# Performance work log

Measured on AMD Instinct MI355X. Metric: run time of the kernel, lower is better.

The kernel has to match this reference:

```python
import jax, jax.numpy as jnp
import numpy as np

N_T = 8
N_R = 2
NOISE = 1e-12  # 10**(-120/10)
B = 65536


def setup_inputs() -> dict:
    key = jax.random.key(0)
    ks = jax.random.split(key, 7)
    return {
        "theta1": jax.random.normal(ks[0], (B, 264), dtype=jnp.float32),
        "G1r": jax.random.normal(ks[1], (B, N_R, 100), dtype=jnp.float32),
        "G1i": jax.random.normal(ks[2], (B, N_R, 100), dtype=jnp.float32),
        "G2r": jax.random.normal(ks[3], (B, N_R, 100), dtype=jnp.float32),
        "G2i": jax.random.normal(ks[4], (B, N_R, 100), dtype=jnp.float32),
        "Ur": jax.random.normal(ks[5], (B, 100, N_T), dtype=jnp.float32),
        "Ui": jax.random.normal(ks[6], (B, 100, N_T), dtype=jnp.float32),
    }


def _rate(phi, Fsig, Fintf):
    # phi: [B, N_r, N_t], Fsig/Fintf: [B, N_t, N_r]
    A = jnp.einsum("bnt,btr->bnr", phi, Fsig)    # signal term  [B, N_r, N_r]
    C = jnp.einsum("bnt,btr->bnr", phi, Fintf)   # interference [B, N_r, N_r]
    # Mu = C C^H + noise (elementwise scalar add, faithful to torch source)
    Mu = jnp.einsum("bnr,bmr->bnm", C, jnp.conj(C)) + NOISE
    inner = jnp.einsum("brn,bnm,bms->brs", jnp.conj(A).transpose(0, 2, 1) if False else jnp.conj(jnp.swapaxes(A, 1, 2)), jnp.linalg.inv(Mu), A)
    # note: torch does 1 + matrix (elementwise), not identity add
    return jnp.real(jnp.log(jnp.linalg.det(1.0 + inner)))  # [B]


def reference(theta1, G1r, G1i, G2r, G2i, Ur, Ui):
    M1N1 = N_T * N_R  # 16
    F1 = theta1[:, 200:200 + M1N1] + 1j * theta1[:, 200 + M1N1:200 + 2 * M1N1]
    F2 = theta1[:, 200 + 2 * M1N1:200 + 3 * M1N1] + 1j * theta1[:, 200 + 3 * M1N1:]
    # power normalization: F * sqrt(2 / (F^H F))
    F1 = F1 * jnp.sqrt(2.0 / jnp.sum(jnp.conj(F1) * F1, axis=1, keepdims=True))
    F2 = F2 * jnp.sqrt(2.0 / jnp.sum(jnp.conj(F2) * F2, axis=1, keepdims=True))
    F1m = F1.reshape(-1, N_T, N_R)
    F2m = F2.reshape(-1, N_T, N_R)

    theta = theta1[:, 0:100] + 1j * theta1[:, 100:200]  # [B, 100]
    G1 = G1r + 1j * G1i
    G2 = G2r + 1j * G2i
    U = Ur + 1j * Ui

    # phi = G @ diag(theta) @ U, vectorized over batch
    phi1 = jnp.einsum("bnk,bk,bkt->bnt", G1, theta, U)  # [B, N_r, N_t]
    phi2 = jnp.einsum("bnk,bk,bkt->bnt", G2, theta, U)

    R1 = _rate(phi1, F1m, F2m)
    R2 = _rate(phi2, F2m, F1m)
    R = jnp.maximum(-R1, -R2)
    return jnp.sum(R) / theta1.shape[0]
```

## Files before the change

kernel.cpp:

```cpp
#include <hip/hip_runtime.h>
#include <math.h>

#define NOISE 1e-12f
#define WSZ 1064
#define WSZ4 266

__device__ __forceinline__ float2 cmul(float2 a, float2 b) {
    return make_float2(a.x*b.x - a.y*b.y, a.x*b.y + a.y*b.x);
}
__device__ __forceinline__ float2 cconjmul(float2 a, float2 b) {
    return make_float2(a.x*b.x + a.y*b.y, a.x*b.y - a.y*b.x);
}
__device__ __forceinline__ float2 cmulconj(float2 a, float2 b) {
    return make_float2(a.x*b.x + a.y*b.y, a.y*b.x - a.x*b.y);
}
__device__ __forceinline__ float2 cadd(float2 a, float2 b){ return make_float2(a.x+b.x, a.y+b.y); }
__device__ __forceinline__ float2 csub(float2 a, float2 b){ return make_float2(a.x-b.x, a.y-b.y); }
__device__ __forceinline__ float2 cscale(float s, float2 a){ return make_float2(s*a.x, s*a.y); }

typedef const void __attribute__((address_space(1)))* gas_t;
typedef void __attribute__((address_space(3)))* las_t;
__device__ __forceinline__ void gll16(const float* g, float* l) {
    __builtin_amdgcn_global_load_lds((gas_t)g, (las_t)l, 16, 0, 0);
}

__global__ __launch_bounds__(256) void rate_kernel(
    const float* __restrict__ t1,
    const float* __restrict__ G1r, const float* __restrict__ G1i,
    const float* __restrict__ G2r, const float* __restrict__ G2i,
    const float* __restrict__ Ur,  const float* __restrict__ Ui,
    float* __restrict__ partial)
{
    __shared__ float4 lds4[4 * 2 * WSZ4];
    __shared__ float2 ent[4][4][16];
    __shared__ float wsum[4];
    const int wave = threadIdx.x >> 6;
    const int lane = threadIdx.x & 63;
    const int t  = lane & 7;
    const int k0 = lane >> 3;
    const int e8 = k0;
    const int nn = (e8 >> 1) & 1;
    const int rr = e8 & 1;
    float* Wbuf = (float*)(lds4 + wave * 2 * WSZ4);

    #define STAGE(dst, bb) {                                                  \
        const float* tb_ = t1 + (long)(bb) * 264;                             \
        gll16(tb_ + lane * 4, (dst));                        \
        if (lane < 2)  gll16(tb_ + 256 + lane * 4, (dst) + 256);              \
        if (lane < 50) {                                                      \
            gll16(G1r + (long)(bb) * 200 + lane * 4, (dst) + 264);            \
            gll16(G1i + (long)(bb) * 200 + lane * 4, (dst) + 464);            \
            gll16(G2r + (long)(bb) * 200 + lane * 4, (dst) + 664);            \
            gll16(G2i + (long)(bb) * 200 + lane * 4, (dst) + 864);            \
        }                                                                     \
    }

    const long bbase = (long)blockIdx.x * 16 + (long)wave * 4;
    STAGE(Wbuf, bbase);

    const float* urb = Ur + bbase * 800;
    const float* uib = Ui + bbase * 800;
    const int uoff = 32 * k0 + t;
    #define LDU2(idx) make_float2(urb[(idx)], uib[(idx)])

    float2 u0 = LDU2(uoff), u1 = LDU2(uoff+8), u2 = LDU2(uoff+16), u3 = LDU2(uoff+24);

    #define CMATH(thr,thi, ar,ai, cr,ci, dr,di, er,ei, u) {      \
        float wr = (thr)*(u).x - (thi)*(u).y;                    \
        float wi = (thr)*(u).y + (thi)*(u).x;                    \
        p[0] += (ar)*wr - (ai)*wi;  p[1] += (ar)*wi + (ai)*wr;   \
        p[2] += (cr)*wr - (ci)*wi;  p[3] += (cr)*wi + (ci)*wr;   \
        p[4] += (dr)*wr - (di)*wi;  p[5] += (dr)*wi + (di)*wr;   \
        p[6] += (er)*wr - (ei)*wi;  p[7] += (er)*wi + (ei)*wr; }

    #define JGROUP(q, U0, U1, U2, U3) {                                   \
        float4 tr  = F4[(q)];        float4 ti  = F4[25  + (q)];          \
        float4 a0r = F4[66  + (q)];  float4 a0i = F4[116 + (q)];          \
        float4 a1r = F4[91  + (q)];  float4 a1i = F4[141 + (q)];          \
        float4 b0r = F4[166 + (q)];  float4 b0i = F4[216 + (q)];          \
        float4 b1r = F4[191 + (q)];  float4 b1i = F4[241 + (q)];          \
        CMATH(tr.x,ti.x, a0r.x,a0i.x, a1r.x,a1i.x, b0r.x,b0i.x, b1r.x,b1i.x, U0); \
        CMATH(tr.y,ti.y, a0r.y,a0i.y, a1r.y,a1i.y, b0r.y,b0i.y, b1r.y,b1i.y, U1); \
        CMATH(tr.z,ti.z, a0r.z,a0i.z, a1r.z,a1i.z, b0r.z,b0i.z, b1r.z,b1i.z, U2); \
        CMATH(tr.w,ti.w, a0r.w,a0i.w, a1r.w,a1i.w, b0r.w,b0i.w, b1r.w,b1i.w, U3); }

    for (int it = 0; it < 4; ++it) {
        float* W = Wbuf + (it & 1) * WSZ;
        const float4* F4 = (const float4*)W;

        if (it < 3) {
            STAGE(Wbuf + ((it + 1) & 1) * WSZ, bbase + it + 1);
            asm volatile("s_waitcnt vmcnt(14)" ::: "memory");
        }
        __builtin_amdgcn_sched_barrier(0);

        float p[8] = {0,0,0,0,0,0,0,0};

        #pragma unroll 1
        for (int j = 0; j < 3; ++j) {
            float2 n0, n1, n2, n3;
            if (j < 2) {
                const int nb = uoff + 256 * (j + 1);
                n0 = LDU2(nb); n1 = LDU2(nb+8); n2 = LDU2(nb+16); n3 = LDU2(nb+24);
            } else {
                n0 = LDU2(768+t); n1 = LDU2(776+t); n2 = LDU2(784+t); n3 = LDU2(792+t);
            }
            JGROUP(k0 + 8*j, u0, u1, u2, u3);
            u0 = n0; u1 = n1; u2 = n2; u3 = n3;
        }
        if (k0 == 0) {
            JGROUP(24, u0, u1, u2, u3);
        }

        if (it < 3) {
            urb += 800; uib += 800;
            u0 = LDU2(uoff); u1 = LDU2(uoff+8); u2 = LDU2(uoff+16); u3 = LDU2(uoff+24);
        }

        #pragma unroll
        for (int q = 0; q < 8; ++q) {
            p[q] += __shfl_xor(p[q], 8);
            p[q] += __shfl_xor(p[q], 32);
        }
        float4 ph;
        {
            float k0r = nn ? p[2] : p[0], s0r = nn ? p[0] : p[2];
            float k0i = nn ? p[3] : p[1], s0i = nn ? p[1] : p[3];
            float k1r = nn ? p[6] : p[4], s1r = nn ? p[4] : p[6];
            float k1i = nn ? p[7] : p[5], s1i = nn ? p[5] : p[7];
            ph.x = k0r + __shfl_xor(s0r, 16);
            ph.y = k0i + __shfl_xor(s0i, 16);
            ph.z = k1r + __shfl_xor(s1r, 16);
            ph.w = k1i + __shfl_xor(s1i, 16);
        }

        float s1, s2;
        {
            int idx = lane & 15;
            int sel = (lane >> 4) & 1;
            float fr = W[200 + sel*32 + idx];
            float fi = W[216 + sel*32 + idx];
            float m = fr*fr + fi*fi;
            #pragma unroll
            for (int s = 1; s < 16; s <<= 1) m += __shfl_xor(m, s);
            float other = __shfl_xor(m, 16);
            float nrm1 = sel ? other : m;
            float nrm2 = sel ? m : other;
            s1 = sqrtf(2.0f / nrm1);
            s2 = sqrtf(2.0f / nrm2);
        }

        {
            int jf = t*2 + rr;
            float2 f1 = make_float2(W[200 + jf], W[216 + jf]);
            float2 f2 = make_float2(W[232 + jf], W[248 + jf]);
            float2 phi1n = make_float2(ph.x, ph.y);
            float2 phi2n = make_float2(ph.z, ph.w);
            bool lo = (e8 < 4);
            float2 E0 = cmul(phi1n, lo ? f1 : f2);
            float2 E1 = cmul(phi2n, lo ? f2 : f1);
            #pragma unroll
            for (int s = 1; s < 8; s <<= 1) {
                E0.x += __shfl_xor(E0.x, s); E0.y += __shfl_xor(E0.y, s);
                E1.x += __shfl_xor(E1.x, s); E1.y += __shfl_xor(E1.y, s);
            }
            if (t == 0) {
                ent[wave][it][e8]     = cscale(lo ? s1 : s2, E0);
                ent[wave][it][e8 + 8] = cscale(lo ? s2 : s1, E1);
            }
        }
    }
    #undef STAGE
    #undef LDU2
    #undef CMATH
    #undef JGROUP
    asm volatile("s_waitcnt lgkmcnt(0)" ::: "memory");
    __builtin_amdgcn_wave_barrier();

    float negR = 0.0f;
    if (lane < 8) {
        const float2* e = &ent[wave][lane >> 1][(lane & 1) * 8];
        float2 A00=e[0], A01=e[1], A10=e[2], A11=e[3];
        float2 C00=e[4], C01=e[5], C10=e[6], C11=e[7];
        float mu00 = C00.x*C00.x + C00.y*C00.y + C01.x*C01.x + C01.y*C01.y + NOISE;
        float mu11 = C10.x*C10.x + C10.y*C10.y + C11.x*C11.x + C11.y*C11.y + NOISE;
        float2 mu01 = cadd(cmulconj(C00, C10), cmulconj(C01, C11));
        mu01.x += NOISE;
        float det = mu00*mu11 - (mu01.x*mu01.x + mu01.y*mu01.y);
        float inv = 1.0f / det;
        float2 mu01c = make_float2(mu01.x, -mu01.y);
        float2 X00 = cscale(inv, csub(cscale(mu11, A00), cmul(mu01,  A10)));
        float2 X01 = cscale(inv, csub(cscale(mu11, A01), cmul(mu01,  A11)));
        float2 X10 = cscale(inv, csub(cscale(mu00, A10), cmul(mu01c, A00)));
        float2 X11 = cscale(inv, csub(cscale(mu00, A11), cmul(mu01c, A01)));
        float2 I00 = cadd(cconjmul(A00, X00), cconjmul(A10, X10));
        float2 I01 = cadd(cconjmul(A00, X01), cconjmul(A10, X11));
        float2 I10 = cadd(cconjmul(A01, X00), cconjmul(A11, X10));
        float2 I11 = cadd(cconjmul(A01, X01), cconjmul(A11, X11));
        I00.x += 1.0f; I01.x += 1.0f; I10.x += 1.0f; I11.x += 1.0f;
        float2 dT = csub(cmul(I00, I11), cmul(I01, I10));
        negR = -0.5f * logf(dT.x*dT.x + dT.y*dT.y);
    }
    float m = fmaxf(negR, __shfl_xor(negR, 1));
    m += __shfl_xor(m, 2);
    m += __shfl_xor(m, 4);
    if (lane == 0) wsum[wave] = m;

    __syncthreads();
    if (threadIdx.x == 0)
        partial[blockIdx.x] = (wsum[0] + wsum[1]) + (wsum[2] + wsum[3]);
}

__global__ __launch_bounds__(256) void reduce_kernel(
    const float* __restrict__ partial, int n, float invB, float* __restrict__ out)
{
    __shared__ float sd[256];
    float s = 0.0f;
    for (int i = threadIdx.x; i < n; i += 256) s += partial[i];
    sd[threadIdx.x] = s;
    __syncthreads();
    for (int o = 128; o > 0; o >>= 1) {
        if ((int)threadIdx.x < o) sd[threadIdx.x] += sd[threadIdx.x + o];
        __syncthreads();
    }
    if (threadIdx.x == 0) out[0] = sd[0] * invB;
}

extern "C" void kernel_launch(void* const* d_in, const int* in_sizes, int n_in,
                              void* d_out, int out_size, void* d_ws, size_t ws_size,
                              hipStream_t stream) {
    const float* t1  = (const float*)d_in[0];
    const float* G1r = (const float*)d_in[1];
    const float* G1i = (const float*)d_in[2];
    const float* G2r = (const float*)d_in[3];
    const float* G2i = (const float*)d_in[4];
    const float* Ur  = (const float*)d_in[5];
    const float* Ui  = (const float*)d_in[6];

    const int B = in_sizes[0] / 264;
    const int nblocks = B / 16;
    float* partial = (float*)d_ws;

    rate_kernel<<<nblocks, 256, 0, stream>>>(t1, G1r, G1i, G2r, G2i, Ur, Ui, partial);
    reduce_kernel<<<1, 256, 0, stream>>>(partial, nblocks, 1.0f / (float)B, (float*)d_out);
}
```

Before: 141.5 us.

## Interleave complex staging in LDS and use packed FP32 complex FMAs

Replaces the direct global-to-LDS async loads with register loads that are written to LDS later in the loop, interleaving real and imaginary parts so each complex value sits in adjacent floats. The inner complex multiply-accumulate now uses inline v_pk_mul_f32/v_pk_fma_f32 on the interleaved pairs, aiming to halve the VALU instruction count of the phi accumulation. The trade-off is extra VGPR pressure from holding the next batch's staged data in registers, plus added LDS write instructions in place of the hardware async path.

```diff
diff --git a/kernel.cpp b/kernel.cpp
--- a/kernel.cpp
+++ b/kernel.cpp
@@ -5,6 +5,23 @@
 #define WSZ 1064
 #define WSZ4 266
 
+typedef float f32x2 __attribute__((ext_vector_type(2)));
+
+__device__ __forceinline__ f32x2 mk2(float x, float y){ f32x2 r; r.x = x; r.y = y; return r; }
+
+__device__ __forceinline__ f32x2 cmul_pk(f32x2 a, f32x2 b) {
+    f32x2 w;
+    asm("v_pk_mul_f32 %0, %1, %2 op_sel:[0,0] op_sel_hi:[0,1]\n\t"
+        "v_pk_fma_f32 %0, %1, %2, %0 op_sel:[1,1,0] op_sel_hi:[1,0,1] neg_lo:[0,1,0]"
+        : "=&v"(w) : "v"(a), "v"(b));
+    return w;
+}
+__device__ __forceinline__ void cfma_pk(f32x2& p, f32x2 a, f32x2 w) {
+    asm("v_pk_fma_f32 %0, %1, %2, %0 op_sel:[0,0,0] op_sel_hi:[0,1,1]\n\t"
+        "v_pk_fma_f32 %0, %1, %2, %0 op_sel:[1,1,0] op_sel_hi:[1,0,1] neg_lo:[0,1,0]"
+        : "+v"(p) : "v"(a), "v"(w));
+}
+
 __device__ __forceinline__ float2 cmul(float2 a, float2 b) {
     return make_float2(a.x*b.x - a.y*b.y, a.x*b.y + a.y*b.x);
 }
@@ -17,12 +34,6 @@
 __device__ __forceinline__ float2 cadd(float2 a, float2 b){ return make_float2(a.x+b.x, a.y+b.y); }
 __device__ __forceinline__ float2 csub(float2 a, float2 b){ return make_float2(a.x-b.x, a.y-b.y); }
 __device__ __forceinline__ float2 cscale(float s, float2 a){ return make_float2(s*a.x, s*a.y); }
-
-typedef const void __attribute__((address_space(1)))* gas_t;
-typedef void __attribute__((address_space(3)))* las_t;
-__device__ __forceinline__ void gll16(const float* g, float* l) {
-    __builtin_amdgcn_global_load_lds((gas_t)g, (las_t)l, 16, 0, 0);
-}
 
 __global__ __launch_bounds__(256) void rate_kernel(
     const float* __restrict__ t1,
@@ -43,73 +54,86 @@
     const int rr = e8 & 1;
     float* Wbuf = (float*)(lds4 + wave * 2 * WSZ4);
 
-    #define STAGE(dst, bb) {                                                  \
+    float4 s_tr, s_ti, s_f, s_ar, s_ai, s_br, s_bi;
+    #define STAGE_LOAD(bb) {                                                  \
         const float* tb_ = t1 + (long)(bb) * 264;                             \
-        gll16(tb_ + lane * 4, (dst));                        \
-        if (lane < 2)  gll16(tb_ + 256 + lane * 4, (dst) + 256);              \
-        if (lane < 50) {                                                      \
-            gll16(G1r + (long)(bb) * 200 + lane * 4, (dst) + 264);            \
-            gll16(G1i + (long)(bb) * 200 + lane * 4, (dst) + 464);            \
-            gll16(G2r + (long)(bb) * 200 + lane * 4, (dst) + 664);            \
-            gll16(G2i + (long)(bb) * 200 + lane * 4, (dst) + 864);            \
-        }                                                                     \
+        if (lane < 25) { s_tr = ((const float4*)tb_)[lane];                   \
+                         s_ti = ((const float4*)(tb_ + 100))[lane]; }         \
+        if (lane < 16)   s_f  = ((const float4*)(tb_ + 200))[lane];           \
+        if (lane < 50) { s_ar = ((const float4*)(G1r + (long)(bb)*200))[lane];\
+                         s_ai = ((const float4*)(G1i + (long)(bb)*200))[lane];\
+                         s_br = ((const float4*)(G2r + (long)(bb)*200))[lane];\
+                         s_bi = ((const float4*)(G2i + (long)(bb)*200))[lane];}\
+    }
+    #define STAGE_WRITE(dst) {                                                \
+        if (lane < 25) { float4* d = (float4*)(dst) + 2*lane;                 \
+            d[0] = make_float4(s_tr.x, s_ti.x, s_tr.y, s_ti.y);               \
+            d[1] = make_float4(s_tr.z, s_ti.z, s_tr.w, s_ti.w); }             \
+        if (lane < 16) ((float4*)((dst) + 200))[lane] = s_f;                  \
+        if (lane < 50) { float4* d = (float4*)((dst) + 264) + 2*lane;         \
+            d[0] = make_float4(s_ar.x, s_ai.x, s_ar.y, s_ai.y);               \
+            d[1] = make_float4(s_ar.z, s_ai.z, s_ar.w, s_ai.w);               \
+            d = (float4*)((dst) + 664) + 2*lane;                              \
+            d[0] = make_float4(s_br.x, s_bi.x, s_br.y, s_bi.y);               \
+            d[1] = make_float4(s_br.z, s_bi.z, s_br.w, s_bi.w); }             \
     }
 
     const long bbase = (long)blockIdx.x * 16 + (long)wave * 4;
-    STAGE(Wbuf, bbase);
+    STAGE_LOAD(bbase);
+    STAGE_WRITE(Wbuf);
 
     const float* urb = Ur + bbase * 800;
     const float* uib = Ui + bbase * 800;
     const int uoff = 32 * k0 + t;
-    #define LDU2(idx) make_float2(urb[(idx)], uib[(idx)])
-
-    float2 u0 = LDU2(uoff), u1 = LDU2(uoff+8), u2 = LDU2(uoff+16), u3 = LDU2(uoff+24);
-
-    #define CMATH(thr,thi, ar,ai, cr,ci, dr,di, er,ei, u) {      \
-        float wr = (thr)*(u).x - (thi)*(u).y;                    \
-        float wi = (thr)*(u).y + (thi)*(u).x;                    \
-        p[0] += (ar)*wr - (ai)*wi;  p[1] += (ar)*wi + (ai)*wr;   \
-        p[2] += (cr)*wr - (ci)*wi;  p[3] += (cr)*wi + (ci)*wr;   \
-        p[4] += (dr)*wr - (di)*wi;  p[5] += (dr)*wi + (di)*wr;   \
-        p[6] += (er)*wr - (ei)*wi;  p[7] += (er)*wi + (ei)*wr; }
-
-    #define JGROUP(q, U0, U1, U2, U3) {                                   \
-        float4 tr  = F4[(q)];        float4 ti  = F4[25  + (q)];          \
-        float4 a0r = F4[66  + (q)];  float4 a0i = F4[116 + (q)];          \
-        float4 a1r = F4[91  + (q)];  float4 a1i = F4[141 + (q)];          \
-        float4 b0r = F4[166 + (q)];  float4 b0i = F4[216 + (q)];          \
-        float4 b1r = F4[191 + (q)];  float4 b1i = F4[241 + (q)];          \
-        CMATH(tr.x,ti.x, a0r.x,a0i.x, a1r.x,a1i.x, b0r.x,b0i.x, b1r.x,b1i.x, U0); \
-        CMATH(tr.y,ti.y, a0r.y,a0i.y, a1r.y,a1i.y, b0r.y,b0i.y, b1r.y,b1i.y, U1); \
-        CMATH(tr.z,ti.z, a0r.z,a0i.z, a1r.z,a1i.z, b0r.z,b0i.z, b1r.z,b1i.z, U2); \
-        CMATH(tr.w,ti.w, a0r.w,a0i.w, a1r.w,a1i.w, b0r.w,b0i.w, b1r.w,b1i.w, U3); }
+    #define LDU2(idx) mk2(urb[(idx)], uib[(idx)])
+
+    f32x2 u0 = LDU2(uoff), u1 = LDU2(uoff+8), u2 = LDU2(uoff+16), u3 = LDU2(uoff+24);
+
+    #define JGROUP_PK(f0, U0, U1, U2, U3) {                                   \
+        float4 t01 = F4[(f0)],      t23 = F4[(f0)+1];                         \
+        float4 a01 = F4[66+(f0)],   a23 = F4[67+(f0)];                        \
+        float4 c01 = F4[116+(f0)],  c23 = F4[117+(f0)];                       \
+        float4 d01 = F4[166+(f0)],  d23 = F4[167+(f0)];                       \
+        float4 e01 = F4[216+(f0)],  e23 = F4[217+(f0)];                       \
+        { f32x2 Wk = cmul_pk(mk2(t01.x,t01.y), U0);                           \
+          cfma_pk(p10, mk2(a01.x,a01.y), Wk); cfma_pk(p11, mk2(c01.x,c01.y), Wk); \
+          cfma_pk(p20, mk2(d01.x,d01.y), Wk); cfma_pk(p21, mk2(e01.x,e01.y), Wk); } \
+        { f32x2 Wk = cmul_pk(mk2(t01.z,t01.w), U1);                           \
+          cfma_pk(p10, mk2(a01.z,a01.w), Wk); cfma_pk(p11, mk2(c01.z,c01.w), Wk); \
+          cfma_pk(p20, mk2(d01.z,d01.w), Wk); cfma_pk(p21, mk2(e01.z,e01.w), Wk); } \
+        { f32x2 Wk = cmul_pk(mk2(t23.x,t23.y), U2);                           \
+          cfma_pk(p10, mk2(a23.x,a23.y), Wk); cfma_pk(p11, mk2(c23.x,c23.y), Wk); \
+          cfma_pk(p20, mk2(d23.x,d23.y), Wk); cfma_pk(p21, mk2(e23.x,e23.y), Wk); } \
+        { f32x2 Wk = cmul_pk(mk2(t23.z,t23.w), U3);                           \
+          cfma_pk(p10, mk2(a23.z,a23.w), Wk); cfma_pk(p11, mk2(c23.z,c23.w), Wk); \
+          cfma_pk(p20, mk2(d23.z,d23.w), Wk); cfma_pk(p21, mk2(e23.z,e23.w), Wk); } }
 
     for (int it = 0; it < 4; ++it) {
         float* W = Wbuf + (it & 1) * WSZ;
         const float4* F4 = (const float4*)W;
 
         if (it < 3) {
-            STAGE(Wbuf + ((it + 1) & 1) * WSZ, bbase + it + 1);
-            asm volatile("s_waitcnt vmcnt(14)" ::: "memory");
-        }
-        __builtin_amdgcn_sched_barrier(0);
-
-        float p[8] = {0,0,0,0,0,0,0,0};
+            STAGE_LOAD(bbase + it + 1);
+            __builtin_amdgcn_sched_barrier(0);
+        }
+
+        f32x2 p10 = mk2(0.f,0.f), p11 = mk2(0.f,0.f);
+        f32x2 p20 = mk2(0.f,0.f), p21 = mk2(0.f,0.f);
 
         #pragma unroll 1
         for (int j = 0; j < 3; ++j) {
-            float2 n0, n1, n2, n3;
+            f32x2 n0, n1, n2, n3;
             if (j < 2) {
                 const int nb = uoff + 256 * (j + 1);
                 n0 = LDU2(nb); n1 = LDU2(nb+8); n2 = LDU2(nb+16); n3 = LDU2(nb+24);
             } else {
                 n0 = LDU2(768+t); n1 = LDU2(776+t); n2 = LDU2(784+t); n3 = LDU2(792+t);
             }
-            JGROUP(k0 + 8*j, u0, u1, u2, u3);
+            JGROUP_PK(2*k0 + 16*j, u0, u1, u2, u3);
             u0 = n0; u1 = n1; u2 = n2; u3 = n3;
         }
         if (k0 == 0) {
-            JGROUP(24, u0, u1, u2, u3);
+            JGROUP_PK(48, u0, u1, u2, u3);
         }
 
         if (it < 3) {
@@ -117,6 +141,7 @@
             u0 = LDU2(uoff); u1 = LDU2(uoff+8); u2 = LDU2(uoff+16); u3 = LDU2(uoff+24);
         }
 
+        float p[8] = {p10.x, p10.y, p11.x, p11.y, p20.x, p20.y, p21.x, p21.y};
         #pragma unroll
         for (int q = 0; q < 8; ++q) {
             p[q] += __shfl_xor(p[q], 8);
@@ -169,11 +194,16 @@
                 ent[wave][it][e8 + 8] = cscale(lo ? s2 : s1, E1);
             }
         }
-    }
-    #undef STAGE
+
+        if (it < 3) {
+            __builtin_amdgcn_sched_barrier(0);
+            STAGE_WRITE(Wbuf + ((it + 1) & 1) * WSZ);
+        }
+    }
+    #undef STAGE_LOAD
+    #undef STAGE_WRITE
     #undef LDU2
-    #undef CMATH
-    #undef JGROUP
+    #undef JGROUP_PK
     asm volatile("s_waitcnt lgkmcnt(0)" ::: "memory");
     __builtin_amdgcn_wave_barrier();
 
```

Measured after the change: 156.0 us. +10.3%, slower.
